# Kernel tuning notes

Hardware: AMD Instinct MI355X
Metric: run time of the kernel (lower is better)

The kernel has to match this reference:

```python
import jax, jax.numpy as jnp
import numpy as np

B, T, D = 16, 2048, 1024
NUM_LAYERS = 4
BN_EPS = 1e-5


def setup_inputs() -> dict:
    key = jax.random.key(0)
    ks = jax.random.split(key, 8)
    s = 1.0 / np.sqrt(D)
    x = jax.random.normal(ks[0], (B, T, D), dtype=jnp.float32)
    Wi = jax.random.normal(ks[1], (D, D), dtype=jnp.float32) * s   # SimpleCell input dense kernel
    bi = jnp.zeros((D,), dtype=jnp.float32)                         # SimpleCell input dense bias
    Wh = jax.random.normal(ks[2], (D, D), dtype=jnp.float32) * s   # recurrent dense kernel (no bias)
    mlp_W = jax.random.normal(ks[3], (NUM_LAYERS, D, D), dtype=jnp.float32) * s
    mlp_b = jnp.zeros((NUM_LAYERS, D), dtype=jnp.float32)
    bn_scale = jnp.ones((NUM_LAYERS, D), dtype=jnp.float32)
    bn_bias = jnp.zeros((NUM_LAYERS, D), dtype=jnp.float32)
    return {"x": x, "Wi": Wi, "bi": bi, "Wh": Wh,
            "mlp_W": mlp_W, "mlp_b": mlp_b,
            "bn_scale": bn_scale, "bn_bias": bn_bias}


def reference(x, Wi, bi, Wh, mlp_W, mlp_b, bn_scale, bn_bias):
    # --- linear recurrence (SimpleCell with identity activation) ---
    # h_t = (x_t @ Wi + bi) + h_{t-1} @ Wh,  h_0 = 0
    xp = jnp.einsum('btd,dh->bth', x, Wi) + bi          # pre-project inputs [B,T,H]

    def step(h, xt):
        h = xt + h @ Wh
        return h, h

    h0 = jnp.zeros((x.shape[0], Wh.shape[0]), dtype=x.dtype)
    _, ys = jax.lax.scan(step, h0, jnp.swapaxes(xp, 0, 1))  # scan over time
    y = jnp.swapaxes(ys, 0, 1)                               # [B,T,H]

    # --- residual MLP stack: gelu(BatchNorm(Linear(y))) + y ---
    n_layers = mlp_W.shape[0]
    for l in range(n_layers):
        z = jnp.einsum('bth,hk->btk', y, mlp_W[l]) + mlp_b[l]
        mean = jnp.mean(z, axis=(0, 1))
        var = jnp.var(z, axis=(0, 1))
        zn = (z - mean) * jax.lax.rsqrt(var + BN_EPS) * bn_scale[l] + bn_bias[l]
        y = jax.nn.gelu(zn) + y
    return y
```

## Files before the change

### kernel.cpp

```cpp
#include <hip/hip_runtime.h>
#include <math.h>

#define Bb   16
#define Tt   2048
#define Dd   1024
#define NL   4
#define MTOT (Bb * Tt)

typedef float f32x4 __attribute__((ext_vector_type(4)));
typedef short bf16x8 __attribute__((ext_vector_type(8)));

__device__ __forceinline__ unsigned short f2bf_rne(float x) {
    unsigned u = __float_as_uint(x);
    u += 0x7fffu + ((u >> 16) & 1u);
    return (unsigned short)(u >> 16);
}
__device__ __forceinline__ float bf2f(unsigned short h) {
    return __uint_as_float(((unsigned)h) << 16);
}
__device__ __forceinline__ float gelu_tanh(float x) {
    float x3 = x * x * x;
    float u  = 0.7978845608028654f * (x + 0.044715f * x3);
    return 0.5f * x * (1.0f + tanhf(u));
}
__device__ __forceinline__ void dma16(const void* g, void* l) {
    __builtin_amdgcn_global_load_lds(
        (const __attribute__((address_space(1))) unsigned int*)g,
        (__attribute__((address_space(3))) unsigned int*)l, 16, 0, 0);
}

__global__ __launch_bounds__(256)
void split_bt(const float* __restrict__ B, short* __restrict__ ht,
              short* __restrict__ lt)
{
    __shared__ float tile[32][33];
    const int t  = threadIdx.x;
    const int r  = t >> 3;
    const int c  = (t & 7) * 4;
    const int kb = blockIdx.y * 32;
    const int nb = blockIdx.x * 32;
    float4 v = *reinterpret_cast<const float4*>(
        &B[(size_t)(kb + r) * Dd + nb + c]);
    tile[r][c + 0] = v.x; tile[r][c + 1] = v.y;
    tile[r][c + 2] = v.z; tile[r][c + 3] = v.w;
    __syncthreads();
    unsigned h[4], lo[4];
#pragma unroll
    for (int q = 0; q < 4; ++q) {
        float f = tile[c + q][r];
        unsigned short hh = f2bf_rne(f);
        float rem = f - bf2f(hh);
        h[q]  = hh;
        lo[q] = f2bf_rne(rem);
    }
    uint2 hw, lw;
    hw.x = h[0]  | (h[1]  << 16); hw.y = h[2]  | (h[3]  << 16);
    lw.x = lo[0] | (lo[1] << 16); lw.y = lo[2] | (lo[3] << 16);
    const int n = nb + r;
    const int s = (c >> 3) ^ ((n >> 1) & 3);
    size_t off = ((size_t)(blockIdx.y * 1024 + n) * 4 + s) * 8 + (c & 4);
    *reinterpret_cast<uint2*>(&ht[off]) = hw;
    *reinterpret_cast<uint2*>(&lt[off]) = lw;
}

template<int MODE, int BN, int NT>
__global__ __launch_bounds__(256, 2)
void mfma_gemm(const float* __restrict__ A,
               const short* __restrict__ Bth, const short* __restrict__ Btl,
               const float* __restrict__ bias,
               const float* __restrict__ Sin,
               float* __restrict__ Cout,
               float* __restrict__ psum, float* __restrict__ psq,
               int m, int tstart)
{
    constexpr int NJ  = NT / 32;
    constexpr int BH  = 10240;
    constexpr int BPL = NT * 32;
    __shared__ __align__(16) short lds[BH + 2 * BPL];
    float* bnF = (float*)lds;

    const int tid  = threadIdx.x;
    const int lane = tid & 63;
    const int w    = tid >> 6;
    const int n0   = blockIdx.x * NT;
    const int m0g  = (MODE == 2) ? (blockIdx.y * Tt + tstart)
                                 : (blockIdx.y * 128);
    const int wm0  = (w >> 1) * 64;
    const int wn0  = (w & 1) * (NT / 2);
    const int ar   = tid >> 3;
    const int ac   = (tid & 7) * 4;

    int  arow_src[4];
    bool avalid[4];
#pragma unroll
    for (int p = 0; p < 4; ++p) {
        int rg = m0g + p * 32 + ar;
        bool v = true;
        if (MODE >= 1) { int t = rg & (Tt - 1); v = (t >= m); }
        avalid[p]   = v;
        arow_src[p] = (MODE >= 1 && v) ? (rg - m) : rg;
    }

    f32x4 acc[4][NJ];
#pragma unroll
    for (int i = 0; i < 4; ++i)
#pragma unroll
        for (int j = 0; j < NJ; ++j) acc[i][j] = (f32x4){0.f, 0.f, 0.f, 0.f};

    int a_off[4];
#pragma unroll
    for (int i = 0; i < 4; ++i) {
        int r = wm0 + i * 16 + (lane & 15);
        a_off[i] = r * 40 + (lane >> 4) * 8;
    }
    const int ln     = lane & 15;
    const int nlb    = wn0 + ln;
    const int b_off0 = BH + nlb * 32 +
                       (((lane >> 4) ^ ((nlb >> 1) & 3)) << 3);

    float4 aReg[4];
#pragma unroll
    for (int p = 0; p < 4; ++p)
        aReg[p] = *reinterpret_cast<const float4*>(
            &A[(size_t)arow_src[p] * Dd + ac]);

    for (int k0 = 0; k0 < Dd; k0 += 32) {
        __syncthreads();
#pragma unroll
        for (int p = 0; p < 4; ++p) {
            float4 v = aReg[p];
            if (MODE >= 1 && !avalid[p]) v = make_float4(0.f, 0.f, 0.f, 0.f);
            int wo = (p * 32 + ar) * 40 + ac;
            unsigned short h0 = f2bf_rne(v.x), h1 = f2bf_rne(v.y),
                           h2 = f2bf_rne(v.z), h3 = f2bf_rne(v.w);
            unsigned short g0 = f2bf_rne(v.x - bf2f(h0)),
                           g1 = f2bf_rne(v.y - bf2f(h1)),
                           g2 = f2bf_rne(v.z - bf2f(h2)),
                           g3 = f2bf_rne(v.w - bf2f(h3));
            uint2 hw, lw;
            hw.x = (unsigned)h0 | ((unsigned)h1 << 16);
            hw.y = (unsigned)h2 | ((unsigned)h3 << 16);
            lw.x = (unsigned)g0 | ((unsigned)g1 << 16);
            lw.y = (unsigned)g2 | ((unsigned)g3 << 16);
            *reinterpret_cast<uint2*>(&lds[wo])        = hw;
            *reinterpret_cast<uint2*>(&lds[wo + 5120]) = lw;
        }
        {
            const int kt = k0 >> 5;
#pragma unroll
            for (int q = 0; q < NT / 64; ++q) {
                size_t gfo = ((size_t)(kt * 1024 + n0 + q * 64 + (tid >> 2))
                              * 4 + (tid & 3)) * 8;
                dma16(&Bth[gfo], &lds[BH + q * 2048 + w * 512]);
                dma16(&Btl[gfo], &lds[BH + BPL + q * 2048 + w * 512]);
            }
        }
        __syncthreads();
        if (k0 + 32 < Dd) {
#pragma unroll
            for (int p = 0; p < 4; ++p)
                aReg[p] = *reinterpret_cast<const float4*>(
                    &A[(size_t)arow_src[p] * Dd + k0 + 32 + ac]);
        }
        bf16x8 ah[4], al[4];
#pragma unroll
        for (int i = 0; i < 4; ++i) {
            ah[i] = *reinterpret_cast<const bf16x8*>(&lds[a_off[i]]);
            al[i] = *reinterpret_cast<const bf16x8*>(&lds[a_off[i] + 5120]);
        }
#pragma unroll
        for (int j = 0; j < NJ; ++j) {
            int bo = b_off0 + j * 512;
            bf16x8 bh = *reinterpret_cast<const bf16x8*>(&lds[bo]);
            bf16x8 bl = *reinterpret_cast<const bf16x8*>(&lds[bo + BPL]);
#pragma unroll
            for (int i = 0; i < 4; ++i) {
                acc[i][j] = __builtin_amdgcn_mfma_f32_16x16x32_bf16(
                    ah[i], bh, acc[i][j], 0, 0, 0);
                acc[i][j] = __builtin_amdgcn_mfma_f32_16x16x32_bf16(
                    ah[i], bl, acc[i][j], 0, 0, 0);
                acc[i][j] = __builtin_amdgcn_mfma_f32_16x16x32_bf16(
                    al[i], bh, acc[i][j], 0, 0, 0);
            }
        }
    }

    if (BN) {
        __syncthreads();
        bnF[tid] = 0.f; bnF[256 + tid] = 0.f;
        __syncthreads();
    }
#pragma unroll
    for (int j = 0; j < NJ; ++j) {
        int cl  = wn0 + j * 16 + (lane & 15);
        int col = n0 + cl;
        float bj = (MODE == 0 && bias) ? bias[col] : 0.f;
        float sv = 0.f, sq = 0.f;
#pragma unroll
        for (int i = 0; i < 4; ++i) {
            int rbase = m0g + wm0 + i * 16 + (lane >> 4) * 4;
#pragma unroll
            for (int e = 0; e < 4; ++e) {
                size_t off = (size_t)(rbase + e) * Dd + col;
                float v = acc[i][j][e] + bj;
                if (MODE >= 1) v += Sin[off];
                Cout[off] = v;
                if (BN) { sv += v; sq += v * v; }
            }
        }
        if (BN) { atomicAdd(&bnF[cl], sv); atomicAdd(&bnF[256 + cl], sq); }
    }
    if (BN) {
        __syncthreads();
        psum[(size_t)blockIdx.y * Dd + n0 + tid] = bnF[tid];
        psq [(size_t)blockIdx.y * Dd + n0 + tid] = bnF[256 + tid];
    }
}

__global__ __launch_bounds__(256)
void bn_stats(const float* __restrict__ ps, const float* __restrict__ pq,
              const float* __restrict__ scale, const float* __restrict__ bias,
              float* __restrict__ Av, float* __restrict__ Cv)
{
    const int d = blockIdx.x * 256 + threadIdx.x;
    float s = 0.f, q = 0.f;
    for (int p = 0; p < 256; ++p) {
        s += ps[p * Dd + d];
        q += pq[p * Dd + d];
    }
    const float invN = 1.0f / 32768.0f;
    float mean = s * invN;
    float var  = q * invN - mean * mean;
    float rs   = rsqrtf(var + 1e-5f);
    float a    = rs * scale[d];
    Av[d] = a;
    Cv[d] = bias[d] - mean * a;
}

__global__ __launch_bounds__(256)
void residual_gelu(const float* __restrict__ Z, const float* __restrict__ Yin,
                   float* __restrict__ Yout,
                   const float* __restrict__ Av, const float* __restrict__ Cv)
{
    const float4* z4 = reinterpret_cast<const float4*>(Z);
    const float4* y4 = reinterpret_cast<const float4*>(Yin);
    float4*       o4 = reinterpret_cast<float4*>(Yout);
    const float4* a4 = reinterpret_cast<const float4*>(Av);
    const float4* c4 = reinterpret_cast<const float4*>(Cv);
    const int n4 = MTOT * Dd / 4;
    for (int i = blockIdx.x * blockDim.x + threadIdx.x; i < n4;
         i += gridDim.x * blockDim.x) {
        int d4 = i & (Dd / 4 - 1);
        float4 z = z4[i], y = y4[i], a = a4[d4], c = c4[d4];
        float4 o;
        o.x = gelu_tanh(fmaf(z.x, a.x, c.x)) + y.x;
        o.y = gelu_tanh(fmaf(z.y, a.y, c.y)) + y.y;
        o.z = gelu_tanh(fmaf(z.z, a.z, c.z)) + y.z;
        o.w = gelu_tanh(fmaf(z.w, a.w, c.w)) + y.w;
        o4[i] = o;
    }
}

extern "C" void kernel_launch(void* const* d_in, const int* in_sizes, int n_in,
                              void* d_out, int out_size, void* d_ws, size_t ws_size,
                              hipStream_t stream)
{
    const float* x    = (const float*)d_in[0];
    const float* Wi   = (const float*)d_in[1];
    const float* bi   = (const float*)d_in[2];
    const float* Wh   = (const float*)d_in[3];
    const float* mlpW = (const float*)d_in[4];
    const float* mlpb = (const float*)d_in[5];
    const float* bns  = (const float*)d_in[6];
    const float* bnb  = (const float*)d_in[7];
    float* out = (float*)d_out;

    float* ws   = (float*)d_ws;
    float* S0   = ws;
    float* Pa   = S0 + (size_t)MTOT * Dd;
    float* Pb   = Pa + (size_t)Dd * Dd;
    float* psum = Pb + (size_t)Dd * Dd;
    float* psq  = psum + 256 * Dd;
    float* abuf = psq + 256 * Dd;
    float* cbuf = abuf + Dd;
    short* Bth  = (short*)(cbuf + Dd);
    short* Btl  = Bth + (size_t)Dd * Dd;

    const dim3 gBig(4, 256);
    const dim3 gSq (8, 8);
    const dim3 gSeq(8, 16);
    const dim3 gBt (32, 32);

#define SPLIT(M) split_bt<<<gBt, 256, 0, stream>>>((M), Bth, Btl)
#define GEMM(MODE, BN, NT, grid, A_, bias_, Sin_, C_, ps_, pq_, m_, ts_)      \
    mfma_gemm<MODE, BN, NT><<<grid, 256, 0, stream>>>(                        \
        (A_), Bth, Btl, (bias_), (Sin_), (C_), (ps_), (pq_), (m_), (ts_))

    SPLIT(Wi);
    GEMM(0, 0, 256, gBig, x, bi, nullptr, S0, nullptr, nullptr, 0, 0);

    SPLIT(Wh);
    GEMM(1, 0, 256, gBig, S0, nullptr, S0, out, nullptr, nullptr, 1, 0);
    GEMM(0, 0, 128, gSq,  Wh, nullptr, nullptr, Pa, nullptr, nullptr, 0, 0);
    SPLIT(Pa);
    GEMM(1, 0, 256, gBig, out, nullptr, out, S0, nullptr, nullptr, 2, 0);
    GEMM(0, 0, 128, gSq,  Pa, nullptr, nullptr, Pb, nullptr, nullptr, 0, 0);
    SPLIT(Pb);
    GEMM(1, 0, 256, gBig, S0, nullptr, S0, out, nullptr, nullptr, 4, 0);
    GEMM(0, 0, 128, gSq,  Pb, nullptr, nullptr, Pa, nullptr, nullptr, 0, 0);
    SPLIT(Pa);
    GEMM(1, 0, 256, gBig, out, nullptr, out, S0, nullptr, nullptr, 8, 0);
    GEMM(0, 0, 128, gSq,  Pa, nullptr, nullptr, Pb, nullptr, nullptr, 0, 0);
    SPLIT(Pb);
    GEMM(1, 0, 256, gBig, S0, nullptr, S0, out, nullptr, nullptr, 16, 0);
    GEMM(0, 0, 128, gSq,  Pb, nullptr, nullptr, Pa, nullptr, nullptr, 0, 0);
    SPLIT(Pa);
    GEMM(1, 0, 256, gBig, out, nullptr, out, S0, nullptr, nullptr, 32, 0);
    GEMM(0, 0, 128, gSq,  Pa, nullptr, nullptr, Pb, nullptr, nullptr, 0, 0);
    SPLIT(Pb);
    GEMM(1, 0, 256, gBig, S0, nullptr, S0, out, nullptr, nullptr, 64, 0);
    GEMM(0, 0, 128, gSq,  Pb, nullptr, nullptr, Pa, nullptr, nullptr, 0, 0);
    SPLIT(Pa);

    for (int i = 1; i < 16; ++i)
        GEMM(2, 0, 128, gSeq, out, nullptr, out, out, nullptr, nullptr,
             128, 128 * i);

    for (int l = 0; l < NL; ++l) {
        SPLIT(mlpW + (size_t)l * Dd * Dd);
        GEMM(0, 1, 256, gBig, out, mlpb + (size_t)l * Dd, nullptr, S0,
             psum, psq, 0, 0);
        bn_stats<<<4, 256, 0, stream>>>(psum, psq, bns + (size_t)l * Dd,
                                        bnb + (size_t)l * Dd, abuf, cbuf);
        residual_gelu<<<2048, 256, 0, stream>>>(S0, out, out, abuf, cbuf);
    }
#undef SPLIT
#undef GEMM
}
```

Measured before the change: 3.789 ms.

## Fuse scan-step and power GEMMs, emit split weights in epilogue, single-pass MLP GEMMs

Merges each log-step scan GEMM with the matching matrix-power GEMM into one launch (fused_ls), whose epilogue writes the bf16 hi/lo split of the new power directly, so the separate split_bt launches go away. All weight splits are hoisted to the start into separate buffers. The MLP GEMMs now use only a single bf16 product (S3=0) instead of the 3-term split, which lowers precision. The A-register prefetch is also removed, giving up that overlap of global loads with compute.

Result: no change. 3.751 ms (-1.0%).

```diff
diff --git a/kernel.cpp b/kernel.cpp
--- a/kernel.cpp
+++ b/kernel.cpp
@@ -63,40 +63,40 @@
     *reinterpret_cast<uint2*>(&lt[off]) = lw;
 }
 
-template<int MODE, int BN, int NT>
-__global__ __launch_bounds__(256, 2)
-void mfma_gemm(const float* __restrict__ A,
-               const short* __restrict__ Bth, const short* __restrict__ Btl,
-               const float* __restrict__ bias,
-               const float* __restrict__ Sin,
-               float* __restrict__ Cout,
-               float* __restrict__ psum, float* __restrict__ psq,
-               int m, int tstart)
-{
-    constexpr int NJ  = NT / 32;
-    constexpr int BH  = 10240;
-    constexpr int BPL = NT * 32;
-    __shared__ __align__(16) short lds[BH + 2 * BPL];
-    float* bnF = (float*)lds;
+template<int MODE, int BN, int NT, int S3, int WSPLIT>
+__device__ __forceinline__ void gemm_body(
+    short* lds, int bx, int by,
+    const float* __restrict__ Af,
+    const short* __restrict__ Bth, const short* __restrict__ Btl,
+    const float* __restrict__ bias,
+    const float* __restrict__ Sin,
+    float* __restrict__ Cf,
+    short* __restrict__ Woh, short* __restrict__ Wol,
+    float* __restrict__ psum, float* __restrict__ psq,
+    int m, int tstart)
+{
+    constexpr int NJ    = NT / 32;
+    constexpr int APL   = 5120;
+    constexpr int BBASE = (S3 ? 2 : 1) * APL;
+    constexpr int BPL   = NT * 32;
 
     const int tid  = threadIdx.x;
     const int lane = tid & 63;
     const int w    = tid >> 6;
-    const int n0   = blockIdx.x * NT;
-    const int m0g  = (MODE == 2) ? (blockIdx.y * Tt + tstart)
-                                 : (blockIdx.y * 128);
+    const int n0   = bx * NT;
+    const int m0g  = (MODE == 2) ? (by * Tt + tstart) : (by * 128);
     const int wm0  = (w >> 1) * 64;
     const int wn0  = (w & 1) * (NT / 2);
+    const int ln   = lane & 15;
     const int ar   = tid >> 3;
     const int ac   = (tid & 7) * 4;
 
-    int  arow_src[4];
-    bool avalid[4];
+    int  arow_src[4]; bool avalid[4];
 #pragma unroll
     for (int p = 0; p < 4; ++p) {
         int rg = m0g + p * 32 + ar;
         bool v = true;
-        if (MODE >= 1) { int t = rg & (Tt - 1); v = (t >= m); }
+        if (MODE == 1) v = ((rg & (Tt - 1)) >= m);
         avalid[p]   = v;
         arow_src[p] = (MODE >= 1 && v) ? (rg - m) : rg;
     }
@@ -109,82 +109,76 @@
 
     int a_off[4];
 #pragma unroll
-    for (int i = 0; i < 4; ++i) {
-        int r = wm0 + i * 16 + (lane & 15);
-        a_off[i] = r * 40 + (lane >> 4) * 8;
-    }
-    const int ln     = lane & 15;
+    for (int i = 0; i < 4; ++i)
+        a_off[i] = (wm0 + i * 16 + ln) * 40 + (lane >> 4) * 8;
     const int nlb    = wn0 + ln;
-    const int b_off0 = BH + nlb * 32 +
+    const int b_off0 = BBASE + nlb * 32 +
                        (((lane >> 4) ^ ((nlb >> 1) & 3)) << 3);
 
-    float4 aReg[4];
-#pragma unroll
-    for (int p = 0; p < 4; ++p)
-        aReg[p] = *reinterpret_cast<const float4*>(
-            &A[(size_t)arow_src[p] * Dd + ac]);
-
-    for (int k0 = 0; k0 < Dd; k0 += 32) {
+    for (int kt = 0; kt < 32; ++kt) {
         __syncthreads();
 #pragma unroll
         for (int p = 0; p < 4; ++p) {
-            float4 v = aReg[p];
-            if (MODE >= 1 && !avalid[p]) v = make_float4(0.f, 0.f, 0.f, 0.f);
+            float4 v = *reinterpret_cast<const float4*>(
+                &Af[(size_t)arow_src[p] * Dd + kt * 32 + ac]);
+            if (MODE == 1 && !avalid[p]) v = make_float4(0.f, 0.f, 0.f, 0.f);
             int wo = (p * 32 + ar) * 40 + ac;
             unsigned short h0 = f2bf_rne(v.x), h1 = f2bf_rne(v.y),
                            h2 = f2bf_rne(v.z), h3 = f2bf_rne(v.w);
-            unsigned short g0 = f2bf_rne(v.x - bf2f(h0)),
-                           g1 = f2bf_rne(v.y - bf2f(h1)),
-                           g2 = f2bf_rne(v.z - bf2f(h2)),
-                           g3 = f2bf_rne(v.w - bf2f(h3));
-            uint2 hw, lw;
+            uint2 hw;
             hw.x = (unsigned)h0 | ((unsigned)h1 << 16);
             hw.y = (unsigned)h2 | ((unsigned)h3 << 16);
-            lw.x = (unsigned)g0 | ((unsigned)g1 << 16);
-            lw.y = (unsigned)g2 | ((unsigned)g3 << 16);
-            *reinterpret_cast<uint2*>(&lds[wo])        = hw;
-            *reinterpret_cast<uint2*>(&lds[wo + 5120]) = lw;
-        }
-        {
-            const int kt = k0 >> 5;
-#pragma unroll
-            for (int q = 0; q < NT / 64; ++q) {
-                size_t gfo = ((size_t)(kt * 1024 + n0 + q * 64 + (tid >> 2))
-                              * 4 + (tid & 3)) * 8;
-                dma16(&Bth[gfo], &lds[BH + q * 2048 + w * 512]);
-                dma16(&Btl[gfo], &lds[BH + BPL + q * 2048 + w * 512]);
+            *reinterpret_cast<uint2*>(&lds[wo]) = hw;
+            if (S3) {
+                unsigned short g0 = f2bf_rne(v.x - bf2f(h0)),
+                               g1 = f2bf_rne(v.y - bf2f(h1)),
+                               g2 = f2bf_rne(v.z - bf2f(h2)),
+                               g3 = f2bf_rne(v.w - bf2f(h3));
+                uint2 lw;
+                lw.x = (unsigned)g0 | ((unsigned)g1 << 16);
+                lw.y = (unsigned)g2 | ((unsigned)g3 << 16);
+                *reinterpret_cast<uint2*>(&lds[wo + APL]) = lw;
             }
         }
-        __syncthreads();
-        if (k0 + 32 < Dd) {
-#pragma unroll
-            for (int p = 0; p < 4; ++p)
-                aReg[p] = *reinterpret_cast<const float4*>(
-                    &A[(size_t)arow_src[p] * Dd + k0 + 32 + ac]);
-        }
+#pragma unroll
+        for (int q = 0; q < NT / 64; ++q) {
+            size_t gfo = ((size_t)(kt * 1024 + n0 + q * 64 + (tid >> 2))
+                          * 4 + (tid & 3)) * 8;
+            dma16(&Bth[gfo], &lds[BBASE + q * 2048 + w * 512]);
+            if (S3)
+                dma16(&Btl[gfo], &lds[BBASE + BPL + q * 2048 + w * 512]);
+        }
+        __syncthreads();
         bf16x8 ah[4], al[4];
 #pragma unroll
         for (int i = 0; i < 4; ++i) {
             ah[i] = *reinterpret_cast<const bf16x8*>(&lds[a_off[i]]);
-            al[i] = *reinterpret_cast<const bf16x8*>(&lds[a_off[i] + 5120]);
+            if (S3)
+                al[i] = *reinterpret_cast<const bf16x8*>(&lds[a_off[i] + APL]);
         }
 #pragma unroll
         for (int j = 0; j < NJ; ++j) {
-            int bo = b_off0 + j * 512;
-            bf16x8 bh = *reinterpret_cast<const bf16x8*>(&lds[bo]);
-            bf16x8 bl = *reinterpret_cast<const bf16x8*>(&lds[bo + BPL]);
-#pragma unroll
-            for (int i = 0; i < 4; ++i) {
+            const bf16x8 bh = *reinterpret_cast<const bf16x8*>(
+                &lds[b_off0 + j * 512]);
+#pragma unroll
+            for (int i = 0; i < 4; ++i)
                 acc[i][j] = __builtin_amdgcn_mfma_f32_16x16x32_bf16(
                     ah[i], bh, acc[i][j], 0, 0, 0);
-                acc[i][j] = __builtin_amdgcn_mfma_f32_16x16x32_bf16(
-                    ah[i], bl, acc[i][j], 0, 0, 0);
-                acc[i][j] = __builtin_amdgcn_mfma_f32_16x16x32_bf16(
-                    al[i], bh, acc[i][j], 0, 0, 0);
+            if (S3) {
+                const bf16x8 bl = *reinterpret_cast<const bf16x8*>(
+                    &lds[b_off0 + j * 512 + BPL]);
+#pragma unroll
+                for (int i = 0; i < 4; ++i) {
+                    acc[i][j] = __builtin_amdgcn_mfma_f32_16x16x32_bf16(
+                        ah[i], bl, acc[i][j], 0, 0, 0);
+                    acc[i][j] = __builtin_amdgcn_mfma_f32_16x16x32_bf16(
+                        al[i], bh, acc[i][j], 0, 0, 0);
+                }
             }
         }
     }
 
+    float* bnF = reinterpret_cast<float*>(lds);
     if (BN) {
         __syncthreads();
         bnF[tid] = 0.f; bnF[256 + tid] = 0.f;
@@ -192,28 +186,89 @@
     }
 #pragma unroll
     for (int j = 0; j < NJ; ++j) {
-        int cl  = wn0 + j * 16 + (lane & 15);
+        int cl  = wn0 + j * 16 + ln;
         int col = n0 + cl;
         float bj = (MODE == 0 && bias) ? bias[col] : 0.f;
         float sv = 0.f, sq = 0.f;
 #pragma unroll
         for (int i = 0; i < 4; ++i) {
             int rbase = m0g + wm0 + i * 16 + (lane >> 4) * 4;
+            float vv[4];
 #pragma unroll
             for (int e = 0; e < 4; ++e) {
                 size_t off = (size_t)(rbase + e) * Dd + col;
                 float v = acc[i][j][e] + bj;
                 if (MODE >= 1) v += Sin[off];
-                Cout[off] = v;
+                Cf[off] = v;
+                vv[e] = v;
                 if (BN) { sv += v; sq += v * v; }
             }
+            if (WSPLIT) {
+                unsigned short h0 = f2bf_rne(vv[0]), h1 = f2bf_rne(vv[1]),
+                               h2 = f2bf_rne(vv[2]), h3 = f2bf_rne(vv[3]);
+                unsigned short l0 = f2bf_rne(vv[0] - bf2f(h0)),
+                               l1 = f2bf_rne(vv[1] - bf2f(h1)),
+                               l2 = f2bf_rne(vv[2] - bf2f(h2)),
+                               l3 = f2bf_rne(vv[3] - bf2f(h3));
+                uint2 hw, lw;
+                hw.x = (unsigned)h0 | ((unsigned)h1 << 16);
+                hw.y = (unsigned)h2 | ((unsigned)h3 << 16);
+                lw.x = (unsigned)l0 | ((unsigned)l1 << 16);
+                lw.y = (unsigned)l2 | ((unsigned)l3 << 16);
+                int kt2 = rbase >> 5;
+                int sl  = (rbase >> 3) & 3;
+                int e0  = rbase & 7;
+                size_t so = ((size_t)(kt2 * 1024 + col) * 4 +
+                             (sl ^ ((col >> 1) & 3))) * 8 + e0;
+                *reinterpret_cast<uint2*>(&Woh[so]) = hw;
+                *reinterpret_cast<uint2*>(&Wol[so]) = lw;
+            }
         }
         if (BN) { atomicAdd(&bnF[cl], sv); atomicAdd(&bnF[256 + cl], sq); }
     }
     if (BN) {
         __syncthreads();
-        psum[(size_t)blockIdx.y * Dd + n0 + tid] = bnF[tid];
-        psq [(size_t)blockIdx.y * Dd + n0 + tid] = bnF[256 + tid];
+        psum[(size_t)by * Dd + n0 + tid] = bnF[tid];
+        psq [(size_t)by * Dd + n0 + tid] = bnF[256 + tid];
+    }
+}
+
+template<int MODE, int BN, int NT, int S3>
+__global__ __launch_bounds__(256, 2)
+void mfma_gemm(const float* __restrict__ Af,
+               const short* __restrict__ Bth, const short* __restrict__ Btl,
+               const float* __restrict__ bias,
+               const float* __restrict__ Sin,
+               float* __restrict__ Cf,
+               float* __restrict__ psum, float* __restrict__ psq,
+               int m, int tstart)
+{
+    constexpr int LSZ = (S3 ? 2 : 1) * (5120 + NT * 32);
+    __shared__ __align__(16) short lds[LSZ];
+    gemm_body<MODE, BN, NT, S3, 0>(lds, blockIdx.x, blockIdx.y,
+                                   Af, Bth, Btl, bias, Sin, Cf,
+                                   nullptr, nullptr, psum, psq, m, tstart);
+}
+
+__global__ __launch_bounds__(256, 2)
+void fused_ls(const float* __restrict__ Sfrom, float* __restrict__ Sto,
+              const float* __restrict__ Pfrom, float* __restrict__ Pto,
+              const short* __restrict__ Bqh, const short* __restrict__ Bql,
+              short* __restrict__ Bqoh, short* __restrict__ Bqol,
+              int m)
+{
+    __shared__ __align__(16) short lds[2 * (5120 + 8192)];
+    if (blockIdx.y < 16) {
+        int sq  = blockIdx.y;
+        int sbx = blockIdx.x + ((sq & 1) << 2);
+        int sby = sq >> 1;
+        gemm_body<0, 0, 128, 1, 1>(lds, sbx, sby, Pfrom, Bqh, Bql,
+                                   nullptr, nullptr, Pto, Bqoh, Bqol,
+                                   nullptr, nullptr, 0, 0);
+    } else {
+        gemm_body<1, 0, 256, 1, 0>(lds, blockIdx.x, blockIdx.y - 16,
+                                   Sfrom, Bqh, Bql, nullptr, Sfrom, Sto,
+                                   nullptr, nullptr, nullptr, nullptr, m, 0);
     }
 }
 
@@ -275,65 +330,57 @@
     const float* bnb  = (const float*)d_in[7];
     float* out = (float*)d_out;
 
+    const size_t NE = (size_t)MTOT * Dd;
+    const size_t MM = (size_t)Dd * Dd;
     float* ws   = (float*)d_ws;
     float* S0   = ws;
-    float* Pa   = S0 + (size_t)MTOT * Dd;
-    float* Pb   = Pa + (size_t)Dd * Dd;
-    float* psum = Pb + (size_t)Dd * Dd;
+    float* Pa   = S0 + NE;
+    float* Pb   = Pa + MM;
+    float* psum = Pb + MM;
     float* psq  = psum + 256 * Dd;
     float* abuf = psq + 256 * Dd;
     float* cbuf = abuf + Dd;
-    short* Bth  = (short*)(cbuf + Dd);
-    short* Btl  = Bth + (size_t)Dd * Dd;
+    short* Bq0h = (short*)(cbuf + Dd);
+    short* Bq0l = Bq0h + MM;
+    short* Bq1h = Bq0l + MM;
+    short* Bq1l = Bq1h + MM;
+    short* BmH[NL]; short* BmL[NL];
+    {
+        short* p = Bq1l + MM;
+        for (int l = 0; l < NL; ++l) { BmH[l] = p; p += MM; BmL[l] = p; p += MM; }
+    }
 
     const dim3 gBig(4, 256);
-    const dim3 gSq (8, 8);
+    const dim3 gF  (4, 272);
     const dim3 gSeq(8, 16);
     const dim3 gBt (32, 32);
 
-#define SPLIT(M) split_bt<<<gBt, 256, 0, stream>>>((M), Bth, Btl)
-#define GEMM(MODE, BN, NT, grid, A_, bias_, Sin_, C_, ps_, pq_, m_, ts_)      \
-    mfma_gemm<MODE, BN, NT><<<grid, 256, 0, stream>>>(                        \
-        (A_), Bth, Btl, (bias_), (Sin_), (C_), (ps_), (pq_), (m_), (ts_))
-
-    SPLIT(Wi);
-    GEMM(0, 0, 256, gBig, x, bi, nullptr, S0, nullptr, nullptr, 0, 0);
-
-    SPLIT(Wh);
-    GEMM(1, 0, 256, gBig, S0, nullptr, S0, out, nullptr, nullptr, 1, 0);
-    GEMM(0, 0, 128, gSq,  Wh, nullptr, nullptr, Pa, nullptr, nullptr, 0, 0);
-    SPLIT(Pa);
-    GEMM(1, 0, 256, gBig, out, nullptr, out, S0, nullptr, nullptr, 2, 0);
-    GEMM(0, 0, 128, gSq,  Pa, nullptr, nullptr, Pb, nullptr, nullptr, 0, 0);
-    SPLIT(Pb);
-    GEMM(1, 0, 256, gBig, S0, nullptr, S0, out, nullptr, nullptr, 4, 0);
-    GEMM(0, 0, 128, gSq,  Pb, nullptr, nullptr, Pa, nullptr, nullptr, 0, 0);
-    SPLIT(Pa);
-    GEMM(1, 0, 256, gBig, out, nullptr, out, S0, nullptr, nullptr, 8, 0);
-    GEMM(0, 0, 128, gSq,  Pa, nullptr, nullptr, Pb, nullptr, nullptr, 0, 0);
-    SPLIT(Pb);
-    GEMM(1, 0, 256, gBig, S0, nullptr, S0, out, nullptr, nullptr, 16, 0);
-    GEMM(0, 0, 128, gSq,  Pb, nullptr, nullptr, Pa, nullptr, nullptr, 0, 0);
-    SPLIT(Pa);
-    GEMM(1, 0, 256, gBig, out, nullptr, out, S0, nullptr, nullptr, 32, 0);
-    GEMM(0, 0, 128, gSq,  Pa, nullptr, nullptr, Pb, nullptr, nullptr, 0, 0);
-    SPLIT(Pb);
-    GEMM(1, 0, 256, gBig, S0, nullptr, S0, out, nullptr, nullptr, 64, 0);
-    GEMM(0, 0, 128, gSq,  Pb, nullptr, nullptr, Pa, nullptr, nullptr, 0, 0);
-    SPLIT(Pa);
+    split_bt<<<gBt, 256, 0, stream>>>(Wi, Bq0h, Bq0l);
+    split_bt<<<gBt, 256, 0, stream>>>(Wh, Bq1h, Bq1l);
+    for (int l = 0; l < NL; ++l)
+        split_bt<<<gBt, 256, 0, stream>>>(mlpW + (size_t)l * MM, BmH[l], BmL[l]);
+
+    mfma_gemm<0, 0, 256, 1><<<gBig, 256, 0, stream>>>(
+        x, Bq0h, Bq0l, bi, nullptr, S0, nullptr, nullptr, 0, 0);
+
+    fused_ls<<<gF, 256, 0, stream>>>(S0, out, Wh, Pa, Bq1h, Bq1l, Bq0h, Bq0l, 1);
+    fused_ls<<<gF, 256, 0, stream>>>(out, S0, Pa, Pb, Bq0h, Bq0l, Bq1h, Bq1l, 2);
+    fused_ls<<<gF, 256, 0, stream>>>(S0, out, Pb, Pa, Bq1h, Bq1l, Bq0h, Bq0l, 4);
+    fused_ls<<<gF, 256, 0, stream>>>(out, S0, Pa, Pb, Bq0h, Bq0l, Bq1h, Bq1l, 8);
+    fused_ls<<<gF, 256, 0, stream>>>(S0, out, Pb, Pa, Bq1h, Bq1l, Bq0h, Bq0l, 16);
+    fused_ls<<<gF, 256, 0, stream>>>(out, S0, Pa, Pb, Bq0h, Bq0l, Bq1h, Bq1l, 32);
+    fused_ls<<<gF, 256, 0, stream>>>(S0, out, Pb, Pa, Bq1h, Bq1l, Bq0h, Bq0l, 64);
 
     for (int i = 1; i < 16; ++i)
-        GEMM(2, 0, 128, gSeq, out, nullptr, out, out, nullptr, nullptr,
-             128, 128 * i);
+        mfma_gemm<2, 0, 128, 1><<<gSeq, 256, 0, stream>>>(
+            out, Bq0h, Bq0l, nullptr, out, out, nullptr, nullptr, 128, 128 * i);
 
     for (int l = 0; l < NL; ++l) {
-        SPLIT(mlpW + (size_t)l * Dd * Dd);
-        GEMM(0, 1, 256, gBig, out, mlpb + (size_t)l * Dd, nullptr, S0,
-             psum, psq, 0, 0);
+        mfma_gemm<0, 1, 256, 0><<<gBig, 256, 0, stream>>>(
+            out, BmH[l], BmL[l], mlpb + (size_t)l * Dd, nullptr, S0,
+            psum, psq, 0, 0);
         bn_stats<<<4, 256, 0, stream>>>(psum, psq, bns + (size_t)l * Dd,
                                         bnb + (size_t)l * Dd, abuf, cbuf);
         residual_gelu<<<2048, 256, 0, stream>>>(S0, out, out, abuf, cbuf);
     }
-#undef SPLIT
-#undef GEMM
-}
+}
```
